# Performance work log

Measured on AMD Instinct MI355X. Metric: run time of the kernel, lower is better.

The kernel has to match this reference:

```python
import jax, jax.numpy as jnp
import numpy as np

B, S_REF, E, H = 128, 2048, 512, 512

def setup_inputs() -> dict:
    key = jax.random.key(0)
    ks = jax.random.split(key, 13)
    def lin(kw, kb, out_d, in_d):
        bound = 1.0 / np.sqrt(in_d)
        w = jax.random.uniform(kw, (out_d, in_d), minval=-bound, maxval=bound, dtype=jnp.float32)
        b = jax.random.uniform(kb, (out_d,), minval=-bound, maxval=bound, dtype=jnp.float32)
        return w, b
    Wa_w, Wa_b = lin(ks[0], ks[1], H, H)
    Ua_w, Ua_b = lin(ks[2], ks[3], H, H)
    Va_w, Va_b = lin(ks[4], ks[5], 1, H)
    Wih_w, Wih_b = lin(ks[6], ks[7], H, E + H)
    Whh_w, Whh_b = lin(ks[8], ks[9], H, H)
    x_t = jax.random.normal(ks[10], (B, 1, E), dtype=jnp.float32)
    x_ref_encoded = jax.random.normal(ks[11], (B, S_REF, H), dtype=jnp.float32)
    h_prev = jax.random.normal(ks[12], (B, H), dtype=jnp.float32)
    return {"x_t": x_t, "x_ref_encoded": x_ref_encoded, "h_prev": h_prev,
            "Wa_w": Wa_w, "Wa_b": Wa_b, "Ua_w": Ua_w, "Ua_b": Ua_b,
            "Va_w": Va_w, "Va_b": Va_b, "Wih_w": Wih_w, "Wih_b": Wih_b,
            "Whh_w": Whh_w, "Whh_b": Whh_b}

def reference(x_t, x_ref_encoded, h_prev, Wa_w, Wa_b, Ua_w, Ua_b, Va_w, Va_b, Wih_w, Wih_b, Whh_w, Whh_b):
    # Bahdanau additive attention
    q = h_prev @ Wa_w.T + Wa_b                      # (B, H)
    k = jnp.einsum('bsh,oh->bso', x_ref_encoded, Ua_w) + Ua_b  # (B, S, H)
    scores = jnp.einsum('bsh,h->bs', jnp.tanh(q[:, None, :] + k), Va_w[0]) + Va_b[0]  # (B, S)
    attn_weights = jax.nn.softmax(scores, axis=1)
    context = jnp.einsum('bs,bsh->bh', attn_weights, x_ref_encoded)  # (B, H)
    # Reservoir RNN cell on concat(x_t[:,0,:], context)
    rnn_in = jnp.concatenate([x_t[:, 0, :], context], axis=1)        # (B, E+H)
    h_next = jnp.tanh(rnn_in @ Wih_w.T + Wih_b + h_prev @ Whh_w.T + Whh_b)
    return (h_next, context)
```

## Files before the change

### kernel.cpp

```cpp
#include <hip/hip_runtime.h>
#include <hip/hip_bf16.h>
#include <math.h>


typedef __attribute__((ext_vector_type(8))) short short8;
typedef __attribute__((ext_vector_type(8))) unsigned short ushort8;
typedef __attribute__((ext_vector_type(4))) float f32x4;

typedef __attribute__((address_space(1))) const unsigned int glob_uint;
typedef __attribute__((address_space(3))) unsigned int lds_uint;

#define S_LEN 2048
#define BDIM 128
#define HDIM 512
#define EDIM 512
#define BM 64
#define BK 128
#define NK (HDIM / BK)
#define NCHUNK (S_LEN / BM)

__device__ __forceinline__ unsigned short f2bf(float f) {
  unsigned int u = __float_as_uint(f);
  u += 0x7fffu + ((u >> 16) & 1u);
  return (unsigned short)(u >> 16);
}

__device__ __forceinline__ float fast_tanh(float x) {
  float e = __expf(2.0f * x);
  return 1.0f - 2.0f / (e + 1.0f);
}

__global__ __launch_bounds__(256) void k_cvt_b(const float* __restrict__ src,
                                               unsigned short* __restrict__ dst) {
  int tid = blockIdx.x * 256 + threadIdx.x;
  int ct = tid >> 10;
  int kt = (tid >> 6) & 15;
  int l = tid & 63;
  int col = ct * 16 + (l & 15);
  int k = kt * 32 + (l >> 4) * 8;
  const float4* s = (const float4*)(src + (size_t)col * HDIM + k);
  float4 v0 = s[0], v1 = s[1];
  ushort8 p;
  p[0] = f2bf(v0.x); p[1] = f2bf(v0.y); p[2] = f2bf(v0.z); p[3] = f2bf(v0.w);
  p[4] = f2bf(v1.x); p[5] = f2bf(v1.y); p[6] = f2bf(v1.z); p[7] = f2bf(v1.w);
  *(ushort8*)(dst + (size_t)tid * 8) = p;
}

__global__ __launch_bounds__(256) void k_q(const float* __restrict__ hp,
                                           const float* __restrict__ Wa,
                                           const float* __restrict__ Wab,
                                           const float* __restrict__ Uab,
                                           float* __restrict__ q) {
  int b = blockIdx.x, oh = blockIdx.y;
  int o = oh * 256 + threadIdx.x;
  __shared__ float hs[HDIM];
  hs[threadIdx.x] = hp[b * HDIM + threadIdx.x];
  hs[threadIdx.x + 256] = hp[b * HDIM + threadIdx.x + 256];
  __syncthreads();
  const float4* wr = (const float4*)(Wa + (size_t)o * HDIM);
  float acc = 0.f;
#pragma unroll 8
  for (int i = 0; i < HDIM / 4; ++i) {
    float4 v = wr[i];
    acc += v.x * hs[i * 4 + 0] + v.y * hs[i * 4 + 1] + v.z * hs[i * 4 + 2] + v.w * hs[i * 4 + 3];
  }
  q[b * HDIM + o] = acc + Wab[o] + Uab[o];
}

__global__ __launch_bounds__(512, 4) void k_scores_ctx(
    const float* __restrict__ xref, const unsigned short* __restrict__ uab,
    const float* __restrict__ q, const float* __restrict__ va,
    float* __restrict__ mArr, float* __restrict__ lArr, float* __restrict__ cpart) {
  int chunk = blockIdx.x;
  int b = blockIdx.y;
  int tid = threadIdx.x;
  int l = tid & 63;
  int w = tid >> 6;

  __shared__ __align__(16) float Af[2][BM * BK];
  __shared__ float sc[BM];
  __shared__ float pl[BM];

  f32x4 acc[4][4];
#pragma unroll
  for (int m = 0; m < 4; ++m)
#pragma unroll
    for (int n = 0; n < 4; ++n) acc[m][n] = f32x4{0.f, 0.f, 0.f, 0.f};

  const float* xb = xref + ((size_t)b * S_LEN + (size_t)chunk * BM) * HDIM;

  int srcoff[4];
#pragma unroll
  for (int i = 0; i < 4; ++i) {
    int s = (w * 4 + i) * 1024 + l * 16;
    int row = s >> 9;
    int kb = (s & 511) ^ ((row & 7) << 4);
    srcoff[i] = row * HDIM + (kb >> 2);
  }

  int lanebase = (((l >> 4) * 32) ^ ((l & 7) << 4));
  int vb0[4];
#pragma unroll
  for (int m = 0; m < 4; ++m) vb0[m] = (m * 16 + (l & 15)) * 512 + lanebase;

#define STAGE(buf, kc)                                                        \
  {                                                                           \
    _Pragma("unroll")                                                         \
    for (int i = 0; i < 4; ++i) {                                             \
      const float* gp = xb + (kc) * BK + srcoff[i];                           \
      float* lp = &Af[buf][(w * 4 + i) * 256];                                \
      __builtin_amdgcn_global_load_lds((glob_uint*)gp, (lds_uint*)lp, 16, 0, 0); \
    }                                                                         \
  }

#define CLUSTER(buf, kc, kk)                                                  \
  {                                                                           \
    short8 afr[4], bfr[4];                                                    \
    _Pragma("unroll")                                                         \
    for (int n = 0; n < 4; ++n) {                                             \
      int ct = w * 4 + n, kt = (kc) * 4 + (kk);                               \
      bfr[n] = *(const short8*)(uab + (((size_t)(ct * 16 + kt) * 64 + l) * 8)); \
    }                                                                         \
    const char* base_ = (const char*)&Af[buf][0];                             \
    _Pragma("unroll")                                                         \
    for (int m = 0; m < 4; ++m) {                                             \
      f32x4 u0 = *(const f32x4*)(base_ + vb0[m] + (kk) * 128);                \
      f32x4 u1 = *(const f32x4*)(base_ + (vb0[m] ^ 16) + (kk) * 128);         \
      union { __hip_bfloat162 h[4]; short8 s; } pk_;                          \
      pk_.h[0] = __float22bfloat162_rn(make_float2(u0[0], u0[1]));            \
      pk_.h[1] = __float22bfloat162_rn(make_float2(u0[2], u0[3]));            \
      pk_.h[2] = __float22bfloat162_rn(make_float2(u1[0], u1[1]));            \
      pk_.h[3] = __float22bfloat162_rn(make_float2(u1[2], u1[3]));            \
      afr[m] = pk_.s;                                                         \
    }                                                                         \
    __builtin_amdgcn_s_setprio(1);                                            \
    _Pragma("unroll")                                                         \
    for (int m = 0; m < 4; ++m)                                               \
      _Pragma("unroll")                                                       \
      for (int n = 0; n < 4; ++n)                                             \
        acc[m][n] = __builtin_amdgcn_mfma_f32_16x16x32_bf16(afr[m], bfr[n],   \
                                                            acc[m][n], 0, 0, 0); \
    __builtin_amdgcn_s_setprio(0);                                            \
  }

#define COMPUTEKC(buf, kc)  \
  CLUSTER(buf, kc, 0) CLUSTER(buf, kc, 1) CLUSTER(buf, kc, 2) CLUSTER(buf, kc, 3)

  STAGE(0, 0);
  if (tid < BM) sc[tid] = 0.f;
  __syncthreads();

  STAGE(1, 1);
  COMPUTEKC(0, 0);
  __syncthreads();

  STAGE(0, 2);
  COMPUTEKC(1, 1);
  __syncthreads();

  STAGE(1, 3);
  COMPUTEKC(0, 2);
  __syncthreads();

  int c = l & 15, g4 = l >> 4;
  float qf[4], vf[4];
#pragma unroll
  for (int n = 0; n < 4; ++n) {
    int o = w * 64 + n * 16 + c;
    qf[n] = q[b * HDIM + o];
    vf[n] = va[o];
  }
  COMPUTEKC(1, 3);

#pragma unroll
  for (int m = 0; m < 4; ++m) {
#pragma unroll
    for (int r = 0; r < 4; ++r) {
      float sum = 0.f;
#pragma unroll
      for (int n = 0; n < 4; ++n) sum += fast_tanh(acc[m][n][r] + qf[n]) * vf[n];
      sum += __shfl_xor(sum, 1);
      sum += __shfl_xor(sum, 2);
      sum += __shfl_xor(sum, 4);
      sum += __shfl_xor(sum, 8);
      if (c == 0) atomicAdd(&sc[m * 16 + g4 * 4 + r], sum);
    }
  }
  __syncthreads();

  float M = sc[l];
#pragma unroll
  for (int off = 32; off >= 1; off >>= 1) M = fmaxf(M, __shfl_xor(M, off));
  float p = __expf(sc[l] - M);
  float lsum = p;
#pragma unroll
  for (int off = 32; off >= 1; off >>= 1) lsum += __shfl_xor(lsum, off);
  if (tid < BM) pl[tid] = p;
  if (tid == 0) {
    mArr[b * NCHUNK + chunk] = M;
    lArr[b * NCHUNK + chunk] = lsum;
  }
  __syncthreads();

  {
    float cacc = 0.f;
#pragma unroll 8
    for (int r = 0; r < BM; ++r) cacc += pl[r] * xb[(size_t)r * HDIM + tid];
    cpart[((size_t)b * NCHUNK + chunk) * HDIM + tid] = cacc;
  }
#undef STAGE
#undef CLUSTER
#undef COMPUTEKC
}

__global__ __launch_bounds__(512) void k_combine(const float* __restrict__ mArr,
                                                 const float* __restrict__ lArr,
                                                 const float* __restrict__ cpart,
                                                 float* __restrict__ ctx,
                                                 float* __restrict__ out_ctx) {
  int b = blockIdx.x, t = threadIdx.x;
  __shared__ float wf[NCHUNK];
  __shared__ float dinv;
  if (t == 0) {
    float M = mArr[b * NCHUNK];
    for (int i = 1; i < NCHUNK; ++i) M = fmaxf(M, mArr[b * NCHUNK + i]);
    float den = 0.f;
    for (int i = 0; i < NCHUNK; ++i) {
      float f = __expf(mArr[b * NCHUNK + i] - M);
      wf[i] = f;
      den += f * lArr[b * NCHUNK + i];
    }
    dinv = 1.0f / den;
  }
  __syncthreads();
  float s = 0.f;
#pragma unroll
  for (int i = 0; i < NCHUNK; ++i) s += wf[i] * cpart[((size_t)b * NCHUNK + i) * HDIM + t];
  float c = s * dinv;
  ctx[b * HDIM + t] = c;
  out_ctx[b * HDIM + t] = c;
}

__global__ __launch_bounds__(256) void k_rnn(const float* __restrict__ xt,
                                             const float* __restrict__ ctx,
                                             const float* __restrict__ hp,
                                             const float* __restrict__ Wih,
                                             const float* __restrict__ Wihb,
                                             const float* __restrict__ Whh,
                                             const float* __restrict__ Whhb,
                                             float* __restrict__ hout) {
  int b = blockIdx.x, oh = blockIdx.y;
  int o = oh * 256 + threadIdx.x;
  __shared__ float xs[EDIM], cs[HDIM], hs[HDIM];
  xs[threadIdx.x] = xt[b * EDIM + threadIdx.x];
  xs[threadIdx.x + 256] = xt[b * EDIM + threadIdx.x + 256];
  cs[threadIdx.x] = ctx[b * HDIM + threadIdx.x];
  cs[threadIdx.x + 256] = ctx[b * HDIM + threadIdx.x + 256];
  hs[threadIdx.x] = hp[b * HDIM + threadIdx.x];
  hs[threadIdx.x + 256] = hp[b * HDIM + threadIdx.x + 256];
  __syncthreads();
  const float4* wi = (const float4*)(Wih + (size_t)o * (EDIM + HDIM));
  float acc = Wihb[o] + Whhb[o];
#pragma unroll 8
  for (int i = 0; i < EDIM / 4; ++i) {
    float4 v = wi[i];
    acc += v.x * xs[i * 4] + v.y * xs[i * 4 + 1] + v.z * xs[i * 4 + 2] + v.w * xs[i * 4 + 3];
  }
  const float4* wi2 = wi + EDIM / 4;
#pragma unroll 8
  for (int i = 0; i < HDIM / 4; ++i) {
    float4 v = wi2[i];
    acc += v.x * cs[i * 4] + v.y * cs[i * 4 + 1] + v.z * cs[i * 4 + 2] + v.w * cs[i * 4 + 3];
  }
  const float4* wh = (const float4*)(Whh + (size_t)o * HDIM);
#pragma unroll 8
  for (int i = 0; i < HDIM / 4; ++i) {
    float4 v = wh[i];
    acc += v.x * hs[i * 4] + v.y * hs[i * 4 + 1] + v.z * hs[i * 4 + 2] + v.w * hs[i * 4 + 3];
  }
  hout[b * HDIM + o] = tanhf(acc);
}

extern "C" void kernel_launch(void* const* d_in, const int* in_sizes, int n_in,
                              void* d_out, int out_size, void* d_ws, size_t ws_size,
                              hipStream_t stream) {
  const float* x_t    = (const float*)d_in[0];
  const float* x_ref  = (const float*)d_in[1];
  const float* h_prev = (const float*)d_in[2];
  const float* Wa_w   = (const float*)d_in[3];
  const float* Wa_b   = (const float*)d_in[4];
  const float* Ua_w   = (const float*)d_in[5];
  const float* Ua_b   = (const float*)d_in[6];
  const float* Va_w   = (const float*)d_in[7];
  const float* Wih_w  = (const float*)d_in[9];
  const float* Wih_b  = (const float*)d_in[10];
  const float* Whh_w  = (const float*)d_in[11];
  const float* Whh_b  = (const float*)d_in[12];

  char* ws = (char*)d_ws;
  unsigned short* ua_fr = (unsigned short*)ws;
  float* q     = (float*)(ws + 524288);
  float* mArr  = (float*)(ws + 786432);
  float* lArr  = (float*)(ws + 802816);
  float* cpart = (float*)(ws + 819200);
  float* ctx   = (float*)(ws + 9207808);

  float* h_out   = (float*)d_out;
  float* ctx_out = h_out + BDIM * HDIM;

  k_cvt_b<<<dim3(128), dim3(256), 0, stream>>>(Ua_w, ua_fr);
  k_q<<<dim3(BDIM, 2), dim3(256), 0, stream>>>(h_prev, Wa_w, Wa_b, Ua_b, q);
  k_scores_ctx<<<dim3(NCHUNK, BDIM), dim3(512), 0, stream>>>(x_ref, ua_fr, q, Va_w, mArr, lArr, cpart);
  k_combine<<<dim3(BDIM), dim3(512), 0, stream>>>(mArr, lArr, cpart, ctx, ctx_out);
  k_rnn<<<dim3(BDIM, 2), dim3(256), 0, stream>>>(x_t, ctx, h_prev, Wih_w, Wih_b, Whh_w, Whh_b, h_out);
}
```

Baseline: 344.4 us.

## Make scores kernel persistent over 16 chunks with bf16 LDS tiles and register prefetch

New measurement: 708.9 us. 2.06x slower.

```diff
diff --git a/kernel.cpp b/kernel.cpp
--- a/kernel.cpp
+++ b/kernel.cpp
@@ -6,23 +6,22 @@
 typedef __attribute__((ext_vector_type(8))) short short8;
 typedef __attribute__((ext_vector_type(8))) unsigned short ushort8;
 typedef __attribute__((ext_vector_type(4))) float f32x4;
-
-typedef __attribute__((address_space(1))) const unsigned int glob_uint;
-typedef __attribute__((address_space(3))) unsigned int lds_uint;
 
 #define S_LEN 2048
 #define BDIM 128
 #define HDIM 512
 #define EDIM 512
 #define BM 64
-#define BK 128
-#define NK (HDIM / BK)
 #define NCHUNK (S_LEN / BM)
 
 __device__ __forceinline__ unsigned short f2bf(float f) {
   unsigned int u = __float_as_uint(f);
   u += 0x7fffu + ((u >> 16) & 1u);
   return (unsigned short)(u >> 16);
+}
+
+__device__ __forceinline__ float bf2f(unsigned short u) {
+  return __uint_as_float(((unsigned int)u) << 16);
 }
 
 __device__ __forceinline__ float fast_tanh(float x) {
@@ -67,150 +66,164 @@
   q[b * HDIM + o] = acc + Wab[o] + Uab[o];
 }
 
-__global__ __launch_bounds__(512, 4) void k_scores_ctx(
+__global__ __launch_bounds__(1024) void k_scores_ctx(
     const float* __restrict__ xref, const unsigned short* __restrict__ uab,
     const float* __restrict__ q, const float* __restrict__ va,
     float* __restrict__ mArr, float* __restrict__ lArr, float* __restrict__ cpart) {
-  int chunk = blockIdx.x;
-  int b = blockIdx.y;
+  int p = blockIdx.x;
+  int b = p >> 1;
+  int chunk0 = (p & 1) * 16;
   int tid = threadIdx.x;
   int l = tid & 63;
   int w = tid >> 6;
-
-  __shared__ __align__(16) float Af[2][BM * BK];
+  int c = l & 15, g4 = l >> 4;
+
+  __shared__ __align__(16) unsigned short As[2][BM * HDIM];
   __shared__ float sc[BM];
   __shared__ float pl[BM];
-
-  f32x4 acc[4][4];
+  __shared__ float s_ctx[HDIM];
+
+  f32x4 acc[4][2];
 #pragma unroll
   for (int m = 0; m < 4; ++m)
 #pragma unroll
-    for (int n = 0; n < 4; ++n) acc[m][n] = f32x4{0.f, 0.f, 0.f, 0.f};
-
-  const float* xb = xref + ((size_t)b * S_LEN + (size_t)chunk * BM) * HDIM;
-
-  int srcoff[4];
-#pragma unroll
-  for (int i = 0; i < 4; ++i) {
-    int s = (w * 4 + i) * 1024 + l * 16;
-    int row = s >> 9;
-    int kb = (s & 511) ^ ((row & 7) << 4);
-    srcoff[i] = row * HDIM + (kb >> 2);
-  }
-
-  int lanebase = (((l >> 4) * 32) ^ ((l & 7) << 4));
-  int vb0[4];
-#pragma unroll
-  for (int m = 0; m < 4; ++m) vb0[m] = (m * 16 + (l & 15)) * 512 + lanebase;
-
-#define STAGE(buf, kc)                                                        \
-  {                                                                           \
-    _Pragma("unroll")                                                         \
-    for (int i = 0; i < 4; ++i) {                                             \
-      const float* gp = xb + (kc) * BK + srcoff[i];                           \
-      float* lp = &Af[buf][(w * 4 + i) * 256];                                \
-      __builtin_amdgcn_global_load_lds((glob_uint*)gp, (lds_uint*)lp, 16, 0, 0); \
-    }                                                                         \
-  }
-
-#define CLUSTER(buf, kc, kk)                                                  \
-  {                                                                           \
-    short8 afr[4], bfr[4];                                                    \
-    _Pragma("unroll")                                                         \
-    for (int n = 0; n < 4; ++n) {                                             \
-      int ct = w * 4 + n, kt = (kc) * 4 + (kk);                               \
-      bfr[n] = *(const short8*)(uab + (((size_t)(ct * 16 + kt) * 64 + l) * 8)); \
-    }                                                                         \
-    const char* base_ = (const char*)&Af[buf][0];                             \
-    _Pragma("unroll")                                                         \
-    for (int m = 0; m < 4; ++m) {                                             \
-      f32x4 u0 = *(const f32x4*)(base_ + vb0[m] + (kk) * 128);                \
-      f32x4 u1 = *(const f32x4*)(base_ + (vb0[m] ^ 16) + (kk) * 128);         \
-      union { __hip_bfloat162 h[4]; short8 s; } pk_;                          \
-      pk_.h[0] = __float22bfloat162_rn(make_float2(u0[0], u0[1]));            \
-      pk_.h[1] = __float22bfloat162_rn(make_float2(u0[2], u0[3]));            \
-      pk_.h[2] = __float22bfloat162_rn(make_float2(u1[0], u1[1]));            \
-      pk_.h[3] = __float22bfloat162_rn(make_float2(u1[2], u1[3]));            \
-      afr[m] = pk_.s;                                                         \
-    }                                                                         \
-    __builtin_amdgcn_s_setprio(1);                                            \
-    _Pragma("unroll")                                                         \
-    for (int m = 0; m < 4; ++m)                                               \
-      _Pragma("unroll")                                                       \
-      for (int n = 0; n < 4; ++n)                                             \
-        acc[m][n] = __builtin_amdgcn_mfma_f32_16x16x32_bf16(afr[m], bfr[n],   \
+    for (int n = 0; n < 2; ++n) acc[m][n] = f32x4{0.f, 0.f, 0.f, 0.f};
+
+  int srow = tid >> 4;
+  int sk = (tid & 15) * 32;
+  float4 g0, g1, g2, g3;
+
+#define ISSUE(i, part)                                                         \
+  {                                                                            \
+    const float4* gp_ = (const float4*)(xref +                                 \
+        ((size_t)b * S_LEN + (size_t)(chunk0 + (i)) * BM + srow) * HDIM +      \
+        sk + (part) * 16);                                                     \
+    g0 = gp_[0]; g1 = gp_[1]; g2 = gp_[2]; g3 = gp_[3];                        \
+  }
+
+#define WRITEP(buf, part)                                                      \
+  {                                                                            \
+    union { __hip_bfloat162 h[4]; ushort8 s; } u0_, u1_;                       \
+    u0_.h[0] = __float22bfloat162_rn(make_float2(g0.x, g0.y));                 \
+    u0_.h[1] = __float22bfloat162_rn(make_float2(g0.z, g0.w));                 \
+    u0_.h[2] = __float22bfloat162_rn(make_float2(g1.x, g1.y));                 \
+    u0_.h[3] = __float22bfloat162_rn(make_float2(g1.z, g1.w));                 \
+    u1_.h[0] = __float22bfloat162_rn(make_float2(g2.x, g2.y));                 \
+    u1_.h[1] = __float22bfloat162_rn(make_float2(g2.z, g2.w));                 \
+    u1_.h[2] = __float22bfloat162_rn(make_float2(g3.x, g3.y));                 \
+    u1_.h[3] = __float22bfloat162_rn(make_float2(g3.z, g3.w));                 \
+    int byte0_ = (tid & 15) * 64 + (part) * 32;                                \
+    char* base_ = (char*)&As[buf][0] + srow * 1024;                            \
+    *(ushort8*)(base_ + ((byte0_) ^ ((srow & 7) << 4))) = u0_.s;               \
+    *(ushort8*)(base_ + ((byte0_ + 16) ^ ((srow & 7) << 4))) = u1_.s;          \
+  }
+
+#define CLUSTER(buf, kt)                                                       \
+  {                                                                            \
+    short8 afr_[4], bfr_[2];                                                   \
+    _Pragma("unroll")                                                          \
+    for (int n = 0; n < 2; ++n) {                                              \
+      int ct = w * 2 + n;                                                      \
+      bfr_[n] = *(const short8*)(uab + (((size_t)(ct * 16 + (kt)) * 64 + l) * 8)); \
+    }                                                                          \
+    _Pragma("unroll")                                                          \
+    for (int m = 0; m < 4; ++m) {                                              \
+      int row = m * 16 + (l & 15);                                             \
+      int kb = ((kt) * 64 + (l >> 4) * 16) ^ ((row & 7) << 4);                 \
+      afr_[m] = *(const short8*)((const char*)&As[buf][0] + row * 1024 + kb);  \
+    }                                                                          \
+    __builtin_amdgcn_s_setprio(1);                                             \
+    _Pragma("unroll")                                                          \
+    for (int m = 0; m < 4; ++m)                                                \
+      _Pragma("unroll")                                                        \
+      for (int n = 0; n < 2; ++n)                                              \
+        acc[m][n] = __builtin_amdgcn_mfma_f32_16x16x32_bf16(afr_[m], bfr_[n],  \
                                                             acc[m][n], 0, 0, 0); \
-    __builtin_amdgcn_s_setprio(0);                                            \
-  }
-
-#define COMPUTEKC(buf, kc)  \
-  CLUSTER(buf, kc, 0) CLUSTER(buf, kc, 1) CLUSTER(buf, kc, 2) CLUSTER(buf, kc, 3)
-
-  STAGE(0, 0);
+    __builtin_amdgcn_s_setprio(0);                                             \
+  }
+
+  float qf[2], vf[2];
+#pragma unroll
+  for (int n = 0; n < 2; ++n) {
+    int o = w * 32 + n * 16 + c;
+    qf[n] = q[b * HDIM + o];
+    vf[n] = va[o];
+  }
+
+  ISSUE(0, 0); WRITEP(0, 0);
+  ISSUE(0, 1); WRITEP(0, 1);
   if (tid < BM) sc[tid] = 0.f;
   __syncthreads();
 
-  STAGE(1, 1);
-  COMPUTEKC(0, 0);
-  __syncthreads();
-
-  STAGE(0, 2);
-  COMPUTEKC(1, 1);
-  __syncthreads();
-
-  STAGE(1, 3);
-  COMPUTEKC(0, 2);
-  __syncthreads();
-
-  int c = l & 15, g4 = l >> 4;
-  float qf[4], vf[4];
-#pragma unroll
-  for (int n = 0; n < 4; ++n) {
-    int o = w * 64 + n * 16 + c;
-    qf[n] = q[b * HDIM + o];
-    vf[n] = va[o];
-  }
-  COMPUTEKC(1, 3);
-
-#pragma unroll
-  for (int m = 0; m < 4; ++m) {
-#pragma unroll
-    for (int r = 0; r < 4; ++r) {
-      float sum = 0.f;
-#pragma unroll
-      for (int n = 0; n < 4; ++n) sum += fast_tanh(acc[m][n][r] + qf[n]) * vf[n];
-      sum += __shfl_xor(sum, 1);
-      sum += __shfl_xor(sum, 2);
-      sum += __shfl_xor(sum, 4);
-      sum += __shfl_xor(sum, 8);
-      if (c == 0) atomicAdd(&sc[m * 16 + g4 * 4 + r], sum);
+  for (int i = 0; i < 16; ++i) {
+    int cur = i & 1, nxt = cur ^ 1;
+    int chunk = chunk0 + i;
+
+    if (i < 15) ISSUE(i + 1, 0);
+    CLUSTER(cur, 0)  CLUSTER(cur, 1)  CLUSTER(cur, 2)  CLUSTER(cur, 3)
+    CLUSTER(cur, 4)  CLUSTER(cur, 5)  CLUSTER(cur, 6)  CLUSTER(cur, 7)
+    if (i < 15) { WRITEP(nxt, 0); ISSUE(i + 1, 1); }
+    CLUSTER(cur, 8)  CLUSTER(cur, 9)  CLUSTER(cur, 10) CLUSTER(cur, 11)
+    CLUSTER(cur, 12) CLUSTER(cur, 13) CLUSTER(cur, 14) CLUSTER(cur, 15)
+    if (i < 15) WRITEP(nxt, 1);
+
+#pragma unroll
+    for (int m = 0; m < 4; ++m) {
+#pragma unroll
+      for (int r = 0; r < 4; ++r) {
+        float sum = 0.f;
+#pragma unroll
+        for (int n = 0; n < 2; ++n) sum += fast_tanh(acc[m][n][r] + qf[n]) * vf[n];
+        sum += __shfl_xor(sum, 1);
+        sum += __shfl_xor(sum, 2);
+        sum += __shfl_xor(sum, 4);
+        sum += __shfl_xor(sum, 8);
+        if (c == 0) atomicAdd(&sc[m * 16 + g4 * 4 + r], sum);
+      }
     }
-  }
-  __syncthreads();
-
-  float M = sc[l];
-#pragma unroll
-  for (int off = 32; off >= 1; off >>= 1) M = fmaxf(M, __shfl_xor(M, off));
-  float p = __expf(sc[l] - M);
-  float lsum = p;
-#pragma unroll
-  for (int off = 32; off >= 1; off >>= 1) lsum += __shfl_xor(lsum, off);
-  if (tid < BM) pl[tid] = p;
-  if (tid == 0) {
-    mArr[b * NCHUNK + chunk] = M;
-    lArr[b * NCHUNK + chunk] = lsum;
-  }
-  __syncthreads();
-
-  {
-    float cacc = 0.f;
-#pragma unroll 8
-    for (int r = 0; r < BM; ++r) cacc += pl[r] * xb[(size_t)r * HDIM + tid];
-    cpart[((size_t)b * NCHUNK + chunk) * HDIM + tid] = cacc;
-  }
-#undef STAGE
+    __syncthreads();
+
+    float M = sc[l];
+#pragma unroll
+    for (int off = 32; off >= 1; off >>= 1) M = fmaxf(M, __shfl_xor(M, off));
+    float pp = __expf(sc[l] - M);
+    float lsum = pp;
+#pragma unroll
+    for (int off = 32; off >= 1; off >>= 1) lsum += __shfl_xor(lsum, off);
+    if (w == 0) pl[l] = pp;
+    if (tid == 0) {
+      mArr[b * NCHUNK + chunk] = M;
+      lArr[b * NCHUNK + chunk] = lsum;
+    }
+    __syncthreads();
+    if (tid < BM) sc[tid] = 0.f;
+
+    {
+      int half = tid >> 9, h = tid & 511;
+      const char* base_ = (const char*)&As[cur][0];
+      float cacc = 0.f;
+#pragma unroll 8
+      for (int rr = 0; rr < 32; ++rr) {
+        int r = half * 32 + rr;
+        int byte = r * 1024 + ((h * 2) ^ ((r & 7) << 4));
+        cacc += pl[r] * bf2f(*(const unsigned short*)(base_ + byte));
+      }
+      if (half == 0) s_ctx[h] = cacc;
+      __syncthreads();
+      if (half == 1)
+        cpart[((size_t)b * NCHUNK + chunk) * HDIM + h] = s_ctx[h] + cacc;
+    }
+
+#pragma unroll
+    for (int m = 0; m < 4; ++m)
+#pragma unroll
+      for (int n = 0; n < 2; ++n) acc[m][n] = f32x4{0.f, 0.f, 0.f, 0.f};
+
+    __syncthreads();
+  }
+#undef ISSUE
+#undef WRITEP
 #undef CLUSTER
-#undef COMPUTEKC
 }
 
 __global__ __launch_bounds__(512) void k_combine(const float* __restrict__ mArr,
@@ -310,7 +323,7 @@
 
   k_cvt_b<<<dim3(128), dim3(256), 0, stream>>>(Ua_w, ua_fr);
   k_q<<<dim3(BDIM, 2), dim3(256), 0, stream>>>(h_prev, Wa_w, Wa_b, Ua_b, q);
-  k_scores_ctx<<<dim3(NCHUNK, BDIM), dim3(512), 0, stream>>>(x_ref, ua_fr, q, Va_w, mArr, lArr, cpart);
+  k_scores_ctx<<<dim3(256), dim3(1024), 0, stream>>>(x_ref, ua_fr, q, Va_w, mArr, lArr, cpart);
   k_combine<<<dim3(BDIM), dim3(512), 0, stream>>>(mArr, lArr, cpart, ctx, ctx_out);
   k_rnn<<<dim3(BDIM, 2), dim3(256), 0, stream>>>(x_t, ctx, h_prev, Wih_w, Wih_b, Whh_w, Whh_b, h_out);
 }
```
